# Kernel tuning notes

Hardware: AMD Instinct MI355X
Metric: run time of the kernel (lower is better)

Reference implementation:

```python
import jax, jax.numpy as jnp
import numpy as np

D = 1024
SCALE = 10.0  # forward does qk.div(1/10) == qk * 10


def setup_inputs() -> dict:
    key = jax.random.key(0)
    ks = jax.random.split(key, 9)
    B, S = 8, 2048
    lim = 1.0 / np.sqrt(D)  # torch Linear default init range
    return {
        "query": jax.random.normal(ks[0], (B, S, D), jnp.float32),
        "key": jax.random.normal(ks[1], (B, S, D), jnp.float32),
        "value": jax.random.normal(ks[2], (B, S, D), jnp.float32),
        "Wq": jax.random.uniform(ks[3], (D, D), jnp.float32, -lim, lim),
        "bq": jax.random.uniform(ks[4], (D,), jnp.float32, -lim, lim),
        "Wk": jax.random.uniform(ks[5], (D, D), jnp.float32, -lim, lim),
        "bk": jax.random.uniform(ks[6], (D,), jnp.float32, -lim, lim),
        "Wv": jax.random.uniform(ks[7], (D, D), jnp.float32, -lim, lim),
        "bv": jax.random.uniform(ks[8], (D,), jnp.float32, -lim, lim),
    }


def reference(query, key, value, Wq, bq, Wk, bk, Wv, bv):
    # torch Linear: x @ W.T + b
    q = jnp.einsum("bsd,ed->bse", query, Wq) + bq
    k = jnp.einsum("bsd,ed->bse", key, Wk) + bk
    v = jnp.einsum("bsd,ed->bse", value, Wv) + bv
    qk = jnp.einsum("bqd,bkd->bqk", q, k)
    scaled_qk = qk * SCALE  # qk.div(1.0 / scale_factor)
    softmax_qk = jax.nn.softmax(scaled_qk, axis=-1)
    # dropout in eval mode == identity (deterministic reference)
    output = jnp.einsum("bqk,bkd->bqd", softmax_qk, v)
    return (output, softmax_qk)
```

## Files before the change

kernel.cpp:

```cpp
#include <hip/hip_runtime.h>

typedef unsigned short u16;
typedef unsigned int u32;
typedef __bf16 bf16x8 __attribute__((ext_vector_type(8)));
typedef float f32x4 __attribute__((ext_vector_type(4)));

__device__ __forceinline__ u16 bf16_rne(float f) {
  u32 u = __float_as_uint(f);
  u += 0x7fffu + ((u >> 16) & 1u);
  return (u16)(u >> 16);
}
__device__ __forceinline__ float bf16_to_f(u16 h) {
  return __uint_as_float(((u32)h) << 16);
}
__device__ __forceinline__ void gload16(const u16* g, u16* l) {
  __builtin_amdgcn_global_load_lds(
      (const __attribute__((address_space(1))) void*)g,
      (__attribute__((address_space(3))) void*)l, 16, 0, 0);
}

__global__ __launch_bounds__(256) void split_kernel(const float* __restrict__ x,
                                                    u16* __restrict__ hi,
                                                    u16* __restrict__ lo, int n8) {
  int i = blockIdx.x * 256 + threadIdx.x;
  if (i >= n8) return;
  float4 a = ((const float4*)x)[2 * i];
  float4 b = ((const float4*)x)[2 * i + 1];
  float v[8] = {a.x, a.y, a.z, a.w, b.x, b.y, b.z, b.w};
  union { u16 u[8]; uint4 q; } H, L;
#pragma unroll
  for (int j = 0; j < 8; ++j) H.u[j] = bf16_rne(v[j]);
  ((uint4*)hi)[i] = H.q;
  if (lo != nullptr) {
#pragma unroll
    for (int j = 0; j < 8; ++j) L.u[j] = bf16_rne(v[j] - bf16_to_f(H.u[j]));
    ((uint4*)lo)[i] = L.q;
  }
}

__global__ __launch_bounds__(256) void split2_kernel(const float* __restrict__ x0,
                                                     u16* __restrict__ hi0,
                                                     u16* __restrict__ lo0,
                                                     const float* __restrict__ x1,
                                                     u16* __restrict__ hi1) {
  int i = blockIdx.x * 256 + threadIdx.x;
  const float* x = blockIdx.z ? x1 : x0;
  u16* hi = blockIdx.z ? hi1 : hi0;
  float4 a = ((const float4*)x)[2 * i];
  float4 b = ((const float4*)x)[2 * i + 1];
  float v[8] = {a.x, a.y, a.z, a.w, b.x, b.y, b.z, b.w};
  union { u16 u[8]; uint4 q; } H, L;
#pragma unroll
  for (int j = 0; j < 8; ++j) H.u[j] = bf16_rne(v[j]);
  ((uint4*)hi)[i] = H.q;
  if (blockIdx.z == 0) {
#pragma unroll
    for (int j = 0; j < 8; ++j) L.u[j] = bf16_rne(v[j] - bf16_to_f(H.u[j]));
    ((uint4*)lo0)[i] = L.q;
  }
}

__global__ __launch_bounds__(256) void splitk_rowdot(const float* __restrict__ X,
                                                     const float* __restrict__ h,
                                                     u16* __restrict__ hi,
                                                     u16* __restrict__ lo,
                                                     float* __restrict__ w) {
  const int t = threadIdx.x, lane = t & 63, wv = t >> 6;
  const size_t row = (size_t)blockIdx.x * 4 + wv;
  const float* xr = X + row * 1024;
  const float4* hf = (const float4*)h;
  float acc = 0.f;
#pragma unroll
  for (int half = 0; half < 2; ++half) {
    const int e0 = half * 512 + lane * 8;
    float4 a = *(const float4*)&xr[e0];
    float4 b = *(const float4*)&xr[e0 + 4];
    float4 ha = hf[e0 >> 2];
    float4 hb = hf[(e0 >> 2) + 1];
    acc += a.x * ha.x + a.y * ha.y + a.z * ha.z + a.w * ha.w +
           b.x * hb.x + b.y * hb.y + b.z * hb.z + b.w * hb.w;
    float v[8] = {a.x, a.y, a.z, a.w, b.x, b.y, b.z, b.w};
    union { u16 u[8]; uint4 q; } H, L;
#pragma unroll
    for (int j = 0; j < 8; ++j) {
      H.u[j] = bf16_rne(v[j]);
      L.u[j] = bf16_rne(v[j] - bf16_to_f(H.u[j]));
    }
    const size_t ci = (row * 1024 + e0) >> 3;
    ((uint4*)hi)[ci] = H.q;
    ((uint4*)lo)[ci] = L.q;
  }
#pragma unroll
  for (int o = 32; o > 0; o >>= 1) acc += __shfl_xor(acc, o, 64);
  if (lane == 0) w[row] = acc;
}

__global__ __launch_bounds__(256) void transpose_split2(
    const float* __restrict__ in0, u16* __restrict__ hiT0, u16* __restrict__ loT0,
    const float* __restrict__ in1, u16* __restrict__ hiT1, u16* __restrict__ loT1) {
  __shared__ float tile[32][33];
  const float* in = blockIdx.z ? in1 : in0;
  u16* hiT = blockIdx.z ? hiT1 : hiT0;
  u16* loT = blockIdx.z ? loT1 : loT0;
  const int t = threadIdx.x;
  const int r0 = blockIdx.y * 32, c0 = blockIdx.x * 32;
  const int x = t & 31, y = t >> 5;
#pragma unroll
  for (int i = 0; i < 4; ++i)
    tile[y + i * 8][x] = in[(size_t)(r0 + y + i * 8) * 1024 + c0 + x];
  __syncthreads();
#pragma unroll
  for (int i = 0; i < 4; ++i) {
    float v = tile[x][y + i * 8];
    u16 h = bf16_rne(v);
    u16 l = bf16_rne(v - bf16_to_f(h));
    size_t o = (size_t)(c0 + y + i * 8) * 1024 + r0 + x;
    hiT[o] = h;
    loT[o] = l;
  }
}

__global__ __launch_bounds__(256) void zero_vec(float* __restrict__ h) {
  h[blockIdx.x * 256 + threadIdx.x] = 0.f;
}

__global__ __launch_bounds__(256) void colvec_kernel(const float* __restrict__ W,
                                                     const float* __restrict__ b,
                                                     float* __restrict__ h) {
  __shared__ float sb[16];
  const int t = threadIdx.x;
  const int e0 = blockIdx.x * 16;
  if (t < 16) sb[t] = b[e0 + t];
  __syncthreads();
  float a0 = 0.f, a1 = 0.f, a2 = 0.f, a3 = 0.f;
#pragma unroll
  for (int i = 0; i < 16; ++i) {
    const float* row = W + (size_t)(e0 + i) * 1024;
    const float be = sb[i];
    a0 += row[t] * be;
    a1 += row[t + 256] * be;
    a2 += row[t + 512] * be;
    a3 += row[t + 768] * be;
  }
  atomicAdd(&h[t], a0);
  atomicAdd(&h[t + 256], a1);
  atomicAdd(&h[t + 512], a2);
  atomicAdd(&h[t + 768], a3);
}

template <int NPROD, int EPI>
__global__ __launch_bounds__(256) void gemm_bt(
    const u16* __restrict__ Ah, const u16* __restrict__ Al,
    const u16* __restrict__ Bh, const u16* __restrict__ Bl,
    const float* __restrict__ bias,
    u16* __restrict__ Ch, u16* __restrict__ Cl,
    float* __restrict__ Cf, float scale, int K,
    int lda, int ldb, int ldc,
    long long batchA, long long batchB, long long batchC) {
  __shared__ u16 sAh[4096];
  __shared__ u16 sBh[4096];
  __shared__ u16 sAl[NPROD == 3 ? 4096 : 64];
  __shared__ u16 sBl[NPROD == 3 ? 4096 : 64];

  const int t = threadIdx.x;
  const int w = t >> 6;
  const int lane = t & 63;
  const int m0 = blockIdx.y * 128;
  const int n0 = blockIdx.x * 128;
  const long long z = blockIdx.z;

  Ah += z * batchA;
  Bh += z * batchB;

  const int rS = t >> 2;
  const int cS = (((t & 3) ^ ((t >> 3) & 3))) * 8;
  const u16* pAh = Ah + (size_t)(m0 + rS) * lda + cS;
  const u16* pBh = Bh + (size_t)(n0 + rS) * ldb + cS;
  const u16* pAl = nullptr;
  const u16* pBl = nullptr;
  if constexpr (NPROD == 3) {
    pAl = Al + z * batchA + (size_t)(m0 + rS) * lda + cS;
    pBl = Bl + z * batchB + (size_t)(n0 + rS) * ldb + cS;
  }

  const int wr = (w >> 1) * 64;
  const int wc = (w & 1) * 64;
  const int fr = lane & 15;
  const int cc = lane >> 4;
  const int fk = (cc ^ ((fr >> 1) & 3)) * 8;

  f32x4 acc[4][4];
#pragma unroll
  for (int i = 0; i < 4; ++i)
#pragma unroll
    for (int j = 0; j < 4; ++j) acc[i][j] = (f32x4){0.f, 0.f, 0.f, 0.f};

  for (int k0 = 0; k0 < K; k0 += 32) {
    __syncthreads();
#pragma unroll
    for (int j = 0; j < 2; ++j) {
      gload16(pAh + (size_t)j * 64 * lda + k0, &sAh[j * 2048 + w * 512]);
      gload16(pBh + (size_t)j * 64 * ldb + k0, &sBh[j * 2048 + w * 512]);
      if constexpr (NPROD == 3) {
        gload16(pAl + (size_t)j * 64 * lda + k0, &sAl[j * 2048 + w * 512]);
        gload16(pBl + (size_t)j * 64 * ldb + k0, &sBl[j * 2048 + w * 512]);
      }
    }
    __syncthreads();
    bf16x8 ah[4], bh[4], al[4], bl[4];
#pragma unroll
    for (int i = 0; i < 4; ++i) {
      ah[i] = *(const bf16x8*)&sAh[(wr + i * 16 + fr) * 32 + fk];
      bh[i] = *(const bf16x8*)&sBh[(wc + i * 16 + fr) * 32 + fk];
      if constexpr (NPROD == 3) {
        al[i] = *(const bf16x8*)&sAl[(wr + i * 16 + fr) * 32 + fk];
        bl[i] = *(const bf16x8*)&sBl[(wc + i * 16 + fr) * 32 + fk];
      }
    }
#pragma unroll
    for (int i = 0; i < 4; ++i)
#pragma unroll
      for (int j = 0; j < 4; ++j) {
        acc[i][j] = __builtin_amdgcn_mfma_f32_16x16x32_bf16(ah[i], bh[j], acc[i][j], 0, 0, 0);
        if constexpr (NPROD == 3) {
          acc[i][j] = __builtin_amdgcn_mfma_f32_16x16x32_bf16(ah[i], bl[j], acc[i][j], 0, 0, 0);
          acc[i][j] = __builtin_amdgcn_mfma_f32_16x16x32_bf16(al[i], bh[j], acc[i][j], 0, 0, 0);
        }
      }
  }

  if constexpr (EPI >= 2) Cf += z * batchC;

#pragma unroll
  for (int i = 0; i < 4; ++i) {
    const int row0 = m0 + wr + i * 16 + ((lane >> 4) << 2);
#pragma unroll
    for (int j = 0; j < 4; ++j) {
      const int col = n0 + wc + j * 16 + (lane & 15);
      if constexpr (EPI == 0) {
        const float b = bias ? bias[col] : 0.0f;
#pragma unroll
        for (int r = 0; r < 4; ++r) {
          float c = acc[i][j][r] + b;
          u16 h = bf16_rne(c);
          u16 l = bf16_rne(c - bf16_to_f(h));
          size_t o = (size_t)(row0 + r) * ldc + col;
          Ch[o] = h;
          Cl[o] = l;
        }
      } else if constexpr (EPI == 1) {
        const float b = bias[col];
        ushort4 pk;
        pk.x = bf16_rne(acc[i][j][0] + b);
        pk.y = bf16_rne(acc[i][j][1] + b);
        pk.z = bf16_rne(acc[i][j][2] + b);
        pk.w = bf16_rne(acc[i][j][3] + b);
        const int bb = row0 >> 11;
        const int s = row0 & 2047;
        *(ushort4*)&Ch[(size_t)bb * 2097152 + (size_t)col * 2048 + s] = pk;
      } else if constexpr (EPI == 2) {
#pragma unroll
        for (int r = 0; r < 4; ++r)
          Cf[(size_t)(row0 + r) * ldc + col] = acc[i][j][r] * scale;
      } else {
        const float wv = bias[(size_t)z * 2048 + col];
#pragma unroll
        for (int r = 0; r < 4; ++r)
          Cf[(size_t)(row0 + r) * ldc + col] = (acc[i][j][r] + wv) * scale;
      }
    }
  }
}

template <int NPROD, int EPI>
__global__ __launch_bounds__(512) void gemm256(
    const u16* __restrict__ Ah, const u16* __restrict__ Al,
    const u16* __restrict__ Bh, const u16* __restrict__ Bl,
    const float* __restrict__ bias,
    u16* __restrict__ Ch, u16* __restrict__ Cl,
    float* __restrict__ Cf, float scale, int K,
    int lda, int ldb, int ldc,
    long long batchA, long long batchB, long long batchC) {
  __shared__ u16 sAh[2][8192];
  __shared__ u16 sBh[2][8192];
  __shared__ u16 sAl[NPROD == 3 ? 16384 : 8];
  __shared__ u16 sBl[NPROD == 3 ? 16384 : 8];

  const int t = threadIdx.x;
  const int w = t >> 6;
  const int lane = t & 63;

  const u32 gx = gridDim.x;
  const u32 gxy = gridDim.x * gridDim.y;
  const u32 total = gxy * gridDim.z;
  const u32 h = blockIdx.x + gridDim.x * (blockIdx.y + gridDim.y * blockIdx.z);
  const u32 l = (h & 7) * (total >> 3) + (h >> 3);
  const u32 bz = l / gxy;
  const u32 rem = l - bz * gxy;
  const u32 by = rem / gx;
  const u32 bx = rem - by * gx;
  const int m0 = by * 256;
  const int n0 = bx * 256;
  const long long z = bz;

  const int rS = t >> 2;
  const int cS = ((t & 3) ^ ((rS >> 1) & 3)) * 8;
  const u16* pAh = Ah + z * batchA + (size_t)(m0 + rS) * lda + cS;
  const u16* pBh = Bh + z * batchB + (size_t)(n0 + rS) * ldb + cS;
  const u16* pAl = nullptr;
  const u16* pBl = nullptr;
  if constexpr (NPROD == 3) {
    pAl = Al + z * batchA + (size_t)(m0 + rS) * lda + cS;
    pBl = Bl + z * batchB + (size_t)(n0 + rS) * ldb + cS;
  }

  const int wr = (w >> 2) * 128;
  const int wc = (w & 3) * 64;
  const int fr = lane & 15;
  const int fk = (((lane >> 4) ^ ((fr >> 1) & 3)) * 8);

  f32x4 acc[8][4];
#pragma unroll
  for (int i = 0; i < 8; ++i)
#pragma unroll
    for (int j = 0; j < 4; ++j) acc[i][j] = (f32x4){0.f, 0.f, 0.f, 0.f};

  auto SAH = [&](int b, int k0) {
    gload16(pAh + k0, &sAh[b][w * 512]);
    gload16(pAh + (size_t)128 * lda + k0, &sAh[b][4096 + w * 512]);
  };
  auto SBH = [&](int b, int k0) {
    gload16(pBh + k0, &sBh[b][w * 512]);
    gload16(pBh + (size_t)128 * ldb + k0, &sBh[b][4096 + w * 512]);
  };
  auto SAL = [&](int b, int k0) {
    gload16(pAl + k0, &sAl[b * 8192 + w * 512]);
    gload16(pAl + (size_t)128 * lda + k0, &sAl[b * 8192 + 4096 + w * 512]);
  };
  auto SBL = [&](int b, int k0) {
    gload16(pBl + k0, &sBl[b * 8192 + w * 512]);
    gload16(pBl + (size_t)128 * ldb + k0, &sBl[b * 8192 + 4096 + w * 512]);
  };

  SAH(0, 0);
  SBH(0, 0);
  if constexpr (NPROD == 3) {
    SAL(0, 0);
    SBL(0, 0);
  }

  const int nt = K >> 5;
  for (int kt = 0; kt < nt; ++kt) {
    const int cur = kt & 1;
    const int nxt = cur ^ 1;
    const bool pf = (kt + 1) < nt;

    if (pf) {
      const int kn = (kt + 1) << 5;
      SAH(nxt, kn);
      SBH(nxt, kn);
      if constexpr (NPROD == 3) {
        SAL(nxt, kn);
        SBL(nxt, kn);
      }
    }
    __builtin_amdgcn_sched_barrier(0);
    if (pf) {
      if constexpr (NPROD == 3)
        asm volatile("s_waitcnt vmcnt(8)" ::: "memory");
      else
        asm volatile("s_waitcnt vmcnt(4)" ::: "memory");
    } else {
      asm volatile("s_waitcnt vmcnt(0)" ::: "memory");
    }
    __builtin_amdgcn_sched_barrier(0);
    asm volatile("s_barrier" ::: "memory");

    if constexpr (NPROD == 3) {
      bf16x8 bh[4], bl[4], a[4][4];
#pragma unroll
      for (int n = 0; n < 4; ++n) {
        bh[n] = *(const bf16x8*)&sBh[cur][(wc + n * 16 + fr) * 32 + fk];
        bl[n] = *(const bf16x8*)&sBl[cur * 8192 + (wc + n * 16 + fr) * 32 + fk];
      }
      a[0][0] = *(const bf16x8*)&sAh[cur][(wr + 0 * 16 + fr) * 32 + fk];
      a[0][1] = *(const bf16x8*)&sAh[cur][(wr + 1 * 16 + fr) * 32 + fk];
      a[0][2] = *(const bf16x8*)&sAl[cur * 8192 + (wr + 0 * 16 + fr) * 32 + fk];
      a[0][3] = *(const bf16x8*)&sAl[cur * 8192 + (wr + 1 * 16 + fr) * 32 + fk];
#pragma unroll
      for (int q = 0; q < 4; ++q) {
        if (q < 3) {
          a[q + 1][0] = *(const bf16x8*)&sAh[cur][(wr + (2 * q + 2) * 16 + fr) * 32 + fk];
          a[q + 1][1] = *(const bf16x8*)&sAh[cur][(wr + (2 * q + 3) * 16 + fr) * 32 + fk];
          a[q + 1][2] = *(const bf16x8*)&sAl[cur * 8192 + (wr + (2 * q + 2) * 16 + fr) * 32 + fk];
          a[q + 1][3] = *(const bf16x8*)&sAl[cur * 8192 + (wr + (2 * q + 3) * 16 + fr) * 32 + fk];
        }
        __builtin_amdgcn_sched_barrier(0);
        if (q < 3)
          asm volatile("s_waitcnt lgkmcnt(4)" ::: "memory");
        else
          asm volatile("s_waitcnt lgkmcnt(0)" ::: "memory");
        __builtin_amdgcn_sched_barrier(0);
        __builtin_amdgcn_s_setprio(1);
#pragma unroll
        for (int n = 0; n < 4; ++n) {
          acc[2 * q][n] = __builtin_amdgcn_mfma_f32_16x16x32_bf16(a[q][0], bh[n], acc[2 * q][n], 0, 0, 0);
          acc[2 * q + 1][n] = __builtin_amdgcn_mfma_f32_16x16x32_bf16(a[q][1], bh[n], acc[2 * q + 1][n], 0, 0, 0);
        }
#pragma unroll
        for (int n = 0; n < 4; ++n) {
          acc[2 * q][n] = __builtin_amdgcn_mfma_f32_16x16x32_bf16(a[q][0], bl[n], acc[2 * q][n], 0, 0, 0);
          acc[2 * q + 1][n] = __builtin_amdgcn_mfma_f32_16x16x32_bf16(a[q][1], bl[n], acc[2 * q + 1][n], 0, 0, 0);
        }
#pragma unroll
        for (int n = 0; n < 4; ++n) {
          acc[2 * q][n] = __builtin_amdgcn_mfma_f32_16x16x32_bf16(a[q][2], bh[n], acc[2 * q][n], 0, 0, 0);
          acc[2 * q + 1][n] = __builtin_amdgcn_mfma_f32_16x16x32_bf16(a[q][3], bh[n], acc[2 * q + 1][n], 0, 0, 0);
        }
        __builtin_amdgcn_s_setprio(0);
        __builtin_amdgcn_sched_barrier(0);
      }
    } else {
      bf16x8 bh[4], a[2][4];
#pragma unroll
      for (int n = 0; n < 4; ++n)
        bh[n] = *(const bf16x8*)&sBh[cur][(wc + n * 16 + fr) * 32 + fk];
#pragma unroll
      for (int i = 0; i < 4; ++i)
        a[0][i] = *(const bf16x8*)&sAh[cur][(wr + i * 16 + fr) * 32 + fk];
#pragma unroll
      for (int q = 0; q < 2; ++q) {
        if (q < 1) {
#pragma unroll
          for (int i = 0; i < 4; ++i)
            a[1][i] = *(const bf16x8*)&sAh[cur][(wr + (4 + i) * 16 + fr) * 32 + fk];
        }
        __builtin_amdgcn_sched_barrier(0);
        if (q < 1)
          asm volatile("s_waitcnt lgkmcnt(4)" ::: "memory");
        else
          asm volatile("s_waitcnt lgkmcnt(0)" ::: "memory");
        __builtin_amdgcn_sched_barrier(0);
        __builtin_amdgcn_s_setprio(1);
#pragma unroll
        for (int i = 0; i < 4; ++i)
#pragma unroll
          for (int n = 0; n < 4; ++n)
            acc[4 * q + i][n] = __builtin_amdgcn_mfma_f32_16x16x32_bf16(a[q][i], bh[n], acc[4 * q + i][n], 0, 0, 0);
        __builtin_amdgcn_s_setprio(0);
        __builtin_amdgcn_sched_barrier(0);
      }
    }

    asm volatile("s_waitcnt lgkmcnt(0)" ::: "memory");
    asm volatile("s_barrier" ::: "memory");
  }

  if constexpr (EPI >= 2) Cf += z * batchC;

#pragma unroll
  for (int i = 0; i < 8; ++i) {
    const int row0 = m0 + wr + i * 16 + ((lane >> 4) << 2);
#pragma unroll
    for (int j = 0; j < 4; ++j) {
      const int col = n0 + wc + j * 16 + (lane & 15);
      if constexpr (EPI == 0) {
        const float bsv = bias ? bias[col] : 0.0f;
#pragma unroll
        for (int r = 0; r < 4; ++r) {
          float c = acc[i][j][r] + bsv;
          u16 hh = bf16_rne(c);
          u16 ll = bf16_rne(c - bf16_to_f(hh));
          size_t o = (size_t)(row0 + r) * ldc + col;
          Ch[o] = hh;
          Cl[o] = ll;
        }
      } else if constexpr (EPI == 1) {
        const float bsv = bias[col];
        ushort4 pk;
        pk.x = bf16_rne(acc[i][j][0] + bsv);
        pk.y = bf16_rne(acc[i][j][1] + bsv);
        pk.z = bf16_rne(acc[i][j][2] + bsv);
        pk.w = bf16_rne(acc[i][j][3] + bsv);
        const int bb = row0 >> 11;
        const int s = row0 & 2047;
        *(ushort4*)&Ch[(size_t)bb * 2097152 + (size_t)col * 2048 + s] = pk;
      } else if constexpr (EPI == 2) {
#pragma unroll
        for (int r = 0; r < 4; ++r)
          Cf[(size_t)(row0 + r) * ldc + col] = acc[i][j][r] * scale;
      } else {
        const float wv = bias[(size_t)z * 2048 + col];
#pragma unroll
        for (int r = 0; r < 4; ++r)
          Cf[(size_t)(row0 + r) * ldc + col] = (acc[i][j][r] + wv) * scale;
      }
    }
  }
}

__global__ __launch_bounds__(256) void softmax_kernel(float* __restrict__ L,
                                                      u16* __restrict__ P) {
  const size_t row = blockIdx.x;
  float* r = L + row * 2048;
  u16* p = P + row * 2048;
  const int t = threadIdx.x;
  const int w = t >> 6;
  const int lane = t & 63;

  float4 v0 = ((const float4*)r)[2 * t];
  float4 v1 = ((const float4*)r)[2 * t + 1];
  float e[8] = {v0.x, v0.y, v0.z, v0.w, v1.x, v1.y, v1.z, v1.w};

  float vm = e[0];
#pragma unroll
  for (int j = 1; j < 8; ++j) vm = fmaxf(vm, e[j]);
#pragma unroll
  for (int o = 32; o > 0; o >>= 1) vm = fmaxf(vm, __shfl_xor(vm, o, 64));
  __shared__ float redm[4], reds[4];
  if (lane == 0) redm[w] = vm;
  __syncthreads();
  vm = fmaxf(fmaxf(redm[0], redm[1]), fmaxf(redm[2], redm[3]));

  float s = 0.f;
#pragma unroll
  for (int j = 0; j < 8; ++j) {
    e[j] = __expf(e[j] - vm);
    s += e[j];
  }
#pragma unroll
  for (int o = 32; o > 0; o >>= 1) s += __shfl_xor(s, o, 64);
  if (lane == 0) reds[w] = s;
  __syncthreads();
  s = reds[0] + reds[1] + reds[2] + reds[3];
  const float inv = 1.0f / s;

  float4 o0, o1;
  o0.x = e[0] * inv; o0.y = e[1] * inv; o0.z = e[2] * inv; o0.w = e[3] * inv;
  o1.x = e[4] * inv; o1.y = e[5] * inv; o1.z = e[6] * inv; o1.w = e[7] * inv;
  ((float4*)r)[2 * t] = o0;
  ((float4*)r)[2 * t + 1] = o1;
  union { u16 u[8]; uint4 q; } pk;
  pk.u[0] = bf16_rne(o0.x); pk.u[1] = bf16_rne(o0.y);
  pk.u[2] = bf16_rne(o0.z); pk.u[3] = bf16_rne(o0.w);
  pk.u[4] = bf16_rne(o1.x); pk.u[5] = bf16_rne(o1.y);
  pk.u[6] = bf16_rne(o1.z); pk.u[7] = bf16_rne(o1.w);
  ((uint4*)p)[t] = pk.q;
}

extern "C" void kernel_launch(void* const* d_in, const int* in_sizes, int n_in,
                              void* d_out, int out_size, void* d_ws, size_t ws_size,
                              hipStream_t stream) {
  const float* Xq = (const float*)d_in[0];
  const float* Xk = (const float*)d_in[1];
  const float* Xv = (const float*)d_in[2];
  const float* Wq = (const float*)d_in[3];
  const float* bq = (const float*)d_in[4];
  const float* Wk = (const float*)d_in[5];
  const float* bk = (const float*)d_in[6];
  const float* Wv = (const float*)d_in[7];
  const float* bv = (const float*)d_in[8];
  (void)bk;

  char* out = (char*)d_out;
  char* ws = (char*)d_ws;

  u16* T_hi = (u16*)(out + 0);
  u16* T_lo = (u16*)(out + 33554432);
  u16* Xq_hi = (u16*)(out + 67108864);
  u16* Xq_lo = (u16*)(out + 100663296);
  u16* Xv_hi = (u16*)(out + 134217728);
  u16* Mt_hi = (u16*)(out + 167772160);
  u16* Mt_lo = (u16*)(out + 171966464);
  float* logits = (float*)(out + 67108864);
  float* outO = (float*)(out + 0);

  u16* WqT_hi = (u16*)(ws + 0);
  u16* WqT_lo = (u16*)(ws + 2097152);
  u16* WkT_hi = (u16*)(ws + 4194304);
  u16* WkT_lo = (u16*)(ws + 6291456);
  u16* Wv_hi = (u16*)(ws + 8388608);
  u16* P = (u16*)(ws + 0);
  float* hvec = (float*)(ws + 67108864);
  float* wvec = (float*)(ws + 67112960);
  u16* Xk_hi = (u16*)(ws + 67178496);
  u16* Xk_lo = (u16*)(ws + 100732928);
  u16* Vt = (u16*)(ws + 134287360);

  transpose_split2<<<dim3(32, 32, 2), 256, 0, stream>>>(
      Wq, WqT_hi, WqT_lo, Wk, WkT_hi, WkT_lo);
  zero_vec<<<4, 256, 0, stream>>>(hvec);
  colvec_kernel<<<64, 256, 0, stream>>>(Wk, bq, hvec);
  split_kernel<<<512, 256, 0, stream>>>(Wv, Wv_hi, nullptr, 131072);

  splitk_rowdot<<<4096, 256, 0, stream>>>(Xk, hvec, Xk_hi, Xk_lo, wvec);
  split2_kernel<<<dim3(8192, 1, 2), 256, 0, stream>>>(
      Xq, Xq_hi, Xq_lo, Xv, Xv_hi);

  gemm_bt<3, 0><<<dim3(8, 8, 1), 256, 0, stream>>>(
      WkT_hi, WkT_lo, WqT_hi, WqT_lo, nullptr, Mt_hi, Mt_lo, nullptr, 1.f,
      1024, 1024, 1024, 1024, 0, 0, 0);
  gemm256<1, 1><<<dim3(4, 64, 1), 512, 0, stream>>>(
      Xv_hi, nullptr, Wv_hi, nullptr, bv, Vt, nullptr, nullptr, 1.f,
      1024, 1024, 1024, 1024, 0, 0, 0);
  gemm256<3, 0><<<dim3(4, 64, 1), 512, 0, stream>>>(
      Xq_hi, Xq_lo, Mt_hi, Mt_lo, nullptr, T_hi, T_lo, nullptr, 1.f,
      1024, 1024, 1024, 1024, 0, 0, 0);
  gemm256<3, 3><<<dim3(8, 8, 8), 512, 0, stream>>>(
      T_hi, T_lo, Xk_hi, Xk_lo, wvec, nullptr, nullptr, logits, 10.f,
      1024, 1024, 1024, 2048, 2048LL * 1024, 2048LL * 1024, 2048LL * 2048);
  softmax_kernel<<<16384, 256, 0, stream>>>(logits, P);
  gemm256<1, 2><<<dim3(4, 8, 8), 512, 0, stream>>>(
      P, nullptr, Vt, nullptr, nullptr, nullptr, nullptr, outO, 1.f,
      2048, 2048, 2048, 1024, 2048LL * 2048, 1024LL * 2048, 2048LL * 1024);
}
```

Before: 871.7 us.

## Use BK=64 tiles for single-product GEMMs and split-K the weight-product GEMM

For the single-product (NPROD=1) path of gemm256, the K tile grows from 32 to 64 with an 8-way XOR swizzle and double-buffered 32KB tiles. This halves the number of barrier/wait rounds per K and issues more MFMAs per sync. Separately, the small 1024x1024 Wk^T·Wq product is split into 4 K-chunks across the grid z dimension, and a new kernel reduces the chunks and splits the result into hi/lo bf16. The split-K change fills more CUs at the cost of an extra fp32 workspace round-trip and one extra launch. The larger tiles raise LDS use per block, which may lower occupancy.

New measurement: 845.1 us. -3.0%, faster.

```diff
diff --git a/kernel.cpp b/kernel.cpp
--- a/kernel.cpp
+++ b/kernel.cpp
@@ -146,6 +146,26 @@
   atomicAdd(&h[t + 256], a1);
   atomicAdd(&h[t + 512], a2);
   atomicAdd(&h[t + 768], a3);
+}
+
+__global__ __launch_bounds__(256) void reduce4_split(const float* __restrict__ S,
+                                                     u16* __restrict__ hi,
+                                                     u16* __restrict__ lo) {
+  const int i = blockIdx.x * 256 + threadIdx.x;
+  float4 s0 = ((const float4*)S)[i];
+  float4 s1 = ((const float4*)(S + 1048576))[i];
+  float4 s2 = ((const float4*)(S + 2097152))[i];
+  float4 s3 = ((const float4*)(S + 3145728))[i];
+  float v[4] = {(s0.x + s1.x) + (s2.x + s3.x), (s0.y + s1.y) + (s2.y + s3.y),
+                (s0.z + s1.z) + (s2.z + s3.z), (s0.w + s1.w) + (s2.w + s3.w)};
+  union { u16 u[4]; ushort4 q; } H, L;
+#pragma unroll
+  for (int j = 0; j < 4; ++j) {
+    H.u[j] = bf16_rne(v[j]);
+    L.u[j] = bf16_rne(v[j] - bf16_to_f(H.u[j]));
+  }
+  ((ushort4*)hi)[i] = H.q;
+  ((ushort4*)lo)[i] = L.q;
 }
 
 template <int NPROD, int EPI>
@@ -281,8 +301,9 @@
     float* __restrict__ Cf, float scale, int K,
     int lda, int ldb, int ldc,
     long long batchA, long long batchB, long long batchC) {
-  __shared__ u16 sAh[2][8192];
-  __shared__ u16 sBh[2][8192];
+  constexpr int TS = (NPROD == 3) ? 8192 : 16384;
+  __shared__ u16 sAh[2 * TS];
+  __shared__ u16 sBh[2 * TS];
   __shared__ u16 sAl[NPROD == 3 ? 16384 : 8];
   __shared__ u16 sBl[NPROD == 3 ? 16384 : 8];
 
@@ -303,8 +324,9 @@
   const int n0 = bx * 256;
   const long long z = bz;
 
-  const int rS = t >> 2;
-  const int cS = ((t & 3) ^ ((rS >> 1) & 3)) * 8;
+  const int rS = (NPROD == 3) ? (t >> 2) : (t >> 3);
+  const int cS = (NPROD == 3) ? (((t & 3) ^ ((rS >> 1) & 3)) * 8)
+                              : (((t & 7) ^ ((rS >> 1) & 7)) * 8);
   const u16* pAh = Ah + z * batchA + (size_t)(m0 + rS) * lda + cS;
   const u16* pBh = Bh + z * batchB + (size_t)(n0 + rS) * ldb + cS;
   const u16* pAl = nullptr;
@@ -318,6 +340,8 @@
   const int wc = (w & 3) * 64;
   const int fr = lane & 15;
   const int fk = (((lane >> 4) ^ ((fr >> 1) & 3)) * 8);
+  const int fk0 = (((lane >> 4) ^ ((fr >> 1) & 7)) * 8);
+  const int fk1 = (((4 + (lane >> 4)) ^ ((fr >> 1) & 7)) * 8);
 
   f32x4 acc[8][4];
 #pragma unroll
@@ -326,12 +350,12 @@
     for (int j = 0; j < 4; ++j) acc[i][j] = (f32x4){0.f, 0.f, 0.f, 0.f};
 
   auto SAH = [&](int b, int k0) {
-    gload16(pAh + k0, &sAh[b][w * 512]);
-    gload16(pAh + (size_t)128 * lda + k0, &sAh[b][4096 + w * 512]);
+    gload16(pAh + k0, &sAh[b * TS + w * 512]);
+    gload16(pAh + (size_t)128 * lda + k0, &sAh[b * TS + 4096 + w * 512]);
   };
   auto SBH = [&](int b, int k0) {
-    gload16(pBh + k0, &sBh[b][w * 512]);
-    gload16(pBh + (size_t)128 * ldb + k0, &sBh[b][4096 + w * 512]);
+    gload16(pBh + k0, &sBh[b * TS + w * 512]);
+    gload16(pBh + (size_t)128 * ldb + k0, &sBh[b * TS + 4096 + w * 512]);
   };
   auto SAL = [&](int b, int k0) {
     gload16(pAl + k0, &sAl[b * 8192 + w * 512]);
@@ -341,57 +365,57 @@
     gload16(pBl + k0, &sBl[b * 8192 + w * 512]);
     gload16(pBl + (size_t)128 * ldb + k0, &sBl[b * 8192 + 4096 + w * 512]);
   };
-
-  SAH(0, 0);
-  SBH(0, 0);
+  auto SAH64 = [&](int b, int k0) {
+#pragma unroll
+    for (int j = 0; j < 4; ++j)
+      gload16(pAh + (size_t)j * 64 * lda + k0, &sAh[b * TS + j * 4096 + w * 512]);
+  };
+  auto SBH64 = [&](int b, int k0) {
+#pragma unroll
+    for (int j = 0; j < 4; ++j)
+      gload16(pBh + (size_t)j * 64 * ldb + k0, &sBh[b * TS + j * 4096 + w * 512]);
+  };
+
   if constexpr (NPROD == 3) {
+    SAH(0, 0);
+    SBH(0, 0);
     SAL(0, 0);
     SBL(0, 0);
-  }
-
-  const int nt = K >> 5;
-  for (int kt = 0; kt < nt; ++kt) {
-    const int cur = kt & 1;
-    const int nxt = cur ^ 1;
-    const bool pf = (kt + 1) < nt;
-
-    if (pf) {
-      const int kn = (kt + 1) << 5;
-      SAH(nxt, kn);
-      SBH(nxt, kn);
-      if constexpr (NPROD == 3) {
+    const int nt = K >> 5;
+    for (int kt = 0; kt < nt; ++kt) {
+      const int cur = kt & 1;
+      const int nxt = cur ^ 1;
+      const bool pf = (kt + 1) < nt;
+      if (pf) {
+        const int kn = (kt + 1) << 5;
+        SAH(nxt, kn);
+        SBH(nxt, kn);
         SAL(nxt, kn);
         SBL(nxt, kn);
       }
-    }
-    __builtin_amdgcn_sched_barrier(0);
-    if (pf) {
-      if constexpr (NPROD == 3)
+      __builtin_amdgcn_sched_barrier(0);
+      if (pf)
         asm volatile("s_waitcnt vmcnt(8)" ::: "memory");
       else
-        asm volatile("s_waitcnt vmcnt(4)" ::: "memory");
-    } else {
-      asm volatile("s_waitcnt vmcnt(0)" ::: "memory");
-    }
-    __builtin_amdgcn_sched_barrier(0);
-    asm volatile("s_barrier" ::: "memory");
-
-    if constexpr (NPROD == 3) {
+        asm volatile("s_waitcnt vmcnt(0)" ::: "memory");
+      __builtin_amdgcn_sched_barrier(0);
+      asm volatile("s_barrier" ::: "memory");
+
       bf16x8 bh[4], bl[4], a[4][4];
 #pragma unroll
       for (int n = 0; n < 4; ++n) {
-        bh[n] = *(const bf16x8*)&sBh[cur][(wc + n * 16 + fr) * 32 + fk];
+        bh[n] = *(const bf16x8*)&sBh[cur * TS + (wc + n * 16 + fr) * 32 + fk];
         bl[n] = *(const bf16x8*)&sBl[cur * 8192 + (wc + n * 16 + fr) * 32 + fk];
       }
-      a[0][0] = *(const bf16x8*)&sAh[cur][(wr + 0 * 16 + fr) * 32 + fk];
-      a[0][1] = *(const bf16x8*)&sAh[cur][(wr + 1 * 16 + fr) * 32 + fk];
+      a[0][0] = *(const bf16x8*)&sAh[cur * TS + (wr + 0 * 16 + fr) * 32 + fk];
+      a[0][1] = *(const bf16x8*)&sAh[cur * TS + (wr + 1 * 16 + fr) * 32 + fk];
       a[0][2] = *(const bf16x8*)&sAl[cur * 8192 + (wr + 0 * 16 + fr) * 32 + fk];
       a[0][3] = *(const bf16x8*)&sAl[cur * 8192 + (wr + 1 * 16 + fr) * 32 + fk];
 #pragma unroll
       for (int q = 0; q < 4; ++q) {
         if (q < 3) {
-          a[q + 1][0] = *(const bf16x8*)&sAh[cur][(wr + (2 * q + 2) * 16 + fr) * 32 + fk];
-          a[q + 1][1] = *(const bf16x8*)&sAh[cur][(wr + (2 * q + 3) * 16 + fr) * 32 + fk];
+          a[q + 1][0] = *(const bf16x8*)&sAh[cur * TS + (wr + (2 * q + 2) * 16 + fr) * 32 + fk];
+          a[q + 1][1] = *(const bf16x8*)&sAh[cur * TS + (wr + (2 * q + 3) * 16 + fr) * 32 + fk];
           a[q + 1][2] = *(const bf16x8*)&sAl[cur * 8192 + (wr + (2 * q + 2) * 16 + fr) * 32 + fk];
           a[q + 1][3] = *(const bf16x8*)&sAl[cur * 8192 + (wr + (2 * q + 3) * 16 + fr) * 32 + fk];
         }
@@ -420,40 +444,65 @@
         __builtin_amdgcn_s_setprio(0);
         __builtin_amdgcn_sched_barrier(0);
       }
-    } else {
-      bf16x8 bh[4], a[2][4];
-#pragma unroll
-      for (int n = 0; n < 4; ++n)
-        bh[n] = *(const bf16x8*)&sBh[cur][(wc + n * 16 + fr) * 32 + fk];
-#pragma unroll
-      for (int i = 0; i < 4; ++i)
-        a[0][i] = *(const bf16x8*)&sAh[cur][(wr + i * 16 + fr) * 32 + fk];
-#pragma unroll
-      for (int q = 0; q < 2; ++q) {
-        if (q < 1) {
-#pragma unroll
-          for (int i = 0; i < 4; ++i)
-            a[1][i] = *(const bf16x8*)&sAh[cur][(wr + (4 + i) * 16 + fr) * 32 + fk];
-        }
-        __builtin_amdgcn_sched_barrier(0);
-        if (q < 1)
-          asm volatile("s_waitcnt lgkmcnt(4)" ::: "memory");
-        else
-          asm volatile("s_waitcnt lgkmcnt(0)" ::: "memory");
-        __builtin_amdgcn_sched_barrier(0);
-        __builtin_amdgcn_s_setprio(1);
-#pragma unroll
-        for (int i = 0; i < 4; ++i)
-#pragma unroll
-          for (int n = 0; n < 4; ++n)
-            acc[4 * q + i][n] = __builtin_amdgcn_mfma_f32_16x16x32_bf16(a[q][i], bh[n], acc[4 * q + i][n], 0, 0, 0);
-        __builtin_amdgcn_s_setprio(0);
-        __builtin_amdgcn_sched_barrier(0);
-      }
+      asm volatile("s_waitcnt lgkmcnt(0)" ::: "memory");
+      asm volatile("s_barrier" ::: "memory");
     }
-
-    asm volatile("s_waitcnt lgkmcnt(0)" ::: "memory");
-    asm volatile("s_barrier" ::: "memory");
+  } else {
+    SAH64(0, 0);
+    SBH64(0, 0);
+    const int nt = K >> 6;
+    for (int kt = 0; kt < nt; ++kt) {
+      const int cur = kt & 1;
+      const int nxt = cur ^ 1;
+      const bool pf = (kt + 1) < nt;
+      if (pf) {
+        const int kn = (kt + 1) << 6;
+        SAH64(nxt, kn);
+        SBH64(nxt, kn);
+      }
+      __builtin_amdgcn_sched_barrier(0);
+      if (pf)
+        asm volatile("s_waitcnt vmcnt(8)" ::: "memory");
+      else
+        asm volatile("s_waitcnt vmcnt(0)" ::: "memory");
+      __builtin_amdgcn_sched_barrier(0);
+      asm volatile("s_barrier" ::: "memory");
+
+      bf16x8 b0[4], b1[4], a0[8], a1[8];
+#pragma unroll
+      for (int n = 0; n < 4; ++n) {
+        b0[n] = *(const bf16x8*)&sBh[cur * TS + (wc + n * 16 + fr) * 64 + fk0];
+        b1[n] = *(const bf16x8*)&sBh[cur * TS + (wc + n * 16 + fr) * 64 + fk1];
+      }
+#pragma unroll
+      for (int i = 0; i < 8; ++i)
+        a0[i] = *(const bf16x8*)&sAh[cur * TS + (wr + i * 16 + fr) * 64 + fk0];
+#pragma unroll
+      for (int i = 0; i < 8; ++i)
+        a1[i] = *(const bf16x8*)&sAh[cur * TS + (wr + i * 16 + fr) * 64 + fk1];
+      __builtin_amdgcn_sched_barrier(0);
+      asm volatile("s_waitcnt lgkmcnt(8)" ::: "memory");
+      __builtin_amdgcn_sched_barrier(0);
+      __builtin_amdgcn_s_setprio(1);
+#pragma unroll
+      for (int i = 0; i < 8; ++i)
+#pragma unroll
+        for (int n = 0; n < 4; ++n)
+          acc[i][n] = __builtin_amdgcn_mfma_f32_16x16x32_bf16(a0[i], b0[n], acc[i][n], 0, 0, 0);
+      __builtin_amdgcn_s_setprio(0);
+      __builtin_amdgcn_sched_barrier(0);
+      asm volatile("s_waitcnt lgkmcnt(0)" ::: "memory");
+      __builtin_amdgcn_sched_barrier(0);
+      __builtin_amdgcn_s_setprio(1);
+#pragma unroll
+      for (int i = 0; i < 8; ++i)
+#pragma unroll
+        for (int n = 0; n < 4; ++n)
+          acc[i][n] = __builtin_amdgcn_mfma_f32_16x16x32_bf16(a1[i], b1[n], acc[i][n], 0, 0, 0);
+      __builtin_amdgcn_s_setprio(0);
+      __builtin_amdgcn_sched_barrier(0);
+      asm volatile("s_barrier" ::: "memory");
+    }
   }
 
   if constexpr (EPI >= 2) Cf += z * batchC;
@@ -580,6 +629,7 @@
   u16* WkT_hi = (u16*)(ws + 4194304);
   u16* WkT_lo = (u16*)(ws + 6291456);
   u16* Wv_hi = (u16*)(ws + 8388608);
+  float* MtS = (float*)(ws + 16777216);
   u16* P = (u16*)(ws + 0);
   float* hvec = (float*)(ws + 67108864);
   float* wvec = (float*)(ws + 67112960);
@@ -597,9 +647,11 @@
   split2_kernel<<<dim3(8192, 1, 2), 256, 0, stream>>>(
       Xq, Xq_hi, Xq_lo, Xv, Xv_hi);
 
-  gemm_bt<3, 0><<<dim3(8, 8, 1), 256, 0, stream>>>(
-      WkT_hi, WkT_lo, WqT_hi, WqT_lo, nullptr, Mt_hi, Mt_lo, nullptr, 1.f,
-      1024, 1024, 1024, 1024, 0, 0, 0);
+  gemm_bt<3, 2><<<dim3(8, 8, 4), 256, 0, stream>>>(
+      WkT_hi, WkT_lo, WqT_hi, WqT_lo, nullptr, nullptr, nullptr, MtS, 1.f,
+      256, 1024, 1024, 1024, 256, 256, 1048576LL);
+  reduce4_split<<<1024, 256, 0, stream>>>(MtS, Mt_hi, Mt_lo);
+
   gemm256<1, 1><<<dim3(4, 64, 1), 512, 0, stream>>>(
       Xv_hi, nullptr, Wv_hi, nullptr, bv, Vt, nullptr, nullptr, 1.f,
       1024, 1024, 1024, 1024, 0, 0, 0);
```
